# Kernel optimization log

Measured on AMD Instinct MI355X. Metric: run time of the kernel, lower is better.

The kernel has to match this reference:

```python
import jax, jax.numpy as jnp
import numpy as np

N_CLASSES = 3

def setup_inputs() -> dict:
    key = jax.random.key(0)
    k1, k2 = jax.random.split(key)
    feats = jax.random.normal(k1, (16, 1024, 1024, 3), dtype=jnp.float32)
    inst = jax.random.randint(k2, (16, 1024, 1024, 1), 0, N_CLASSES, dtype=jnp.int32)
    return {"feats": feats, "inst": inst}

def reference(feats, inst):
    # Faithful to the TF layer: for each class c, compute the GLOBAL mean of
    # feats over all masked elements (mask tiled across the 3 channels, over
    # the whole batch), then scatter that scalar back into masked positions.
    # Class masks are disjoint, so the sequential update order is benign.
    for c in range(N_CLASSES):
        mask = (inst == c)                                   # [B,H,W,1]
        maskb = jnp.broadcast_to(mask, feats.shape)          # [B,H,W,3]
        cnt = jnp.sum(maskb.astype(feats.dtype))             # scalar count (incl. channels)
        feats_mean = jnp.sum(jnp.where(maskb, feats, 0)) / cnt
        feats = jnp.where(maskb, feats_mean, feats)
    return feats
```

## Files before the change

kernel.cpp:

```cpp
#include <hip/hip_runtime.h>


#define RBLK 1024

__device__ inline double wred_d(double v) {
#pragma unroll
    for (int off = 32; off; off >>= 1) v += __shfl_down(v, off, 64);
    return v;
}
__device__ inline unsigned wred_u(unsigned v) {
#pragma unroll
    for (int off = 32; off; off >>= 1) v += __shfl_down(v, off, 64);
    return v;
}

__global__ __launch_bounds__(256) void reduce_k(const float* __restrict__ feats,
                                                const int* __restrict__ inst,
                                                double* __restrict__ psum,
                                                unsigned* __restrict__ pcnt,
                                                int npix4) {
    int tid = blockIdx.x * 256 + threadIdx.x;
    int stride = gridDim.x * 256;
    double s0 = 0.0, s1 = 0.0, s2 = 0.0;
    unsigned c0 = 0, c1 = 0, c2 = 0;
    const int4* inst4 = (const int4*)inst;
    for (int i = tid; i < npix4; i += stride) {
        int4 cls = inst4[i];
        const float4* f = (const float4*)(feats + (size_t)i * 12);
        float4 a = f[0], b = f[1], c = f[2];
        double d0 = (double)(a.x + a.y + a.z);
        double d1 = (double)(a.w + b.x + b.y);
        double d2 = (double)(b.z + b.w + c.x);
        double d3 = (double)(c.y + c.z + c.w);
        s0 += (cls.x == 0) ? d0 : 0.0;
        s1 += (cls.x == 1) ? d0 : 0.0;
        s2 += (cls.x == 2) ? d0 : 0.0;
        s0 += (cls.y == 0) ? d1 : 0.0;
        s1 += (cls.y == 1) ? d1 : 0.0;
        s2 += (cls.y == 2) ? d1 : 0.0;
        s0 += (cls.z == 0) ? d2 : 0.0;
        s1 += (cls.z == 1) ? d2 : 0.0;
        s2 += (cls.z == 2) ? d2 : 0.0;
        s0 += (cls.w == 0) ? d3 : 0.0;
        s1 += (cls.w == 1) ? d3 : 0.0;
        s2 += (cls.w == 2) ? d3 : 0.0;
        c0 += (unsigned)(cls.x == 0) + (unsigned)(cls.y == 0) +
              (unsigned)(cls.z == 0) + (unsigned)(cls.w == 0);
        c1 += (unsigned)(cls.x == 1) + (unsigned)(cls.y == 1) +
              (unsigned)(cls.z == 1) + (unsigned)(cls.w == 1);
        c2 += (unsigned)(cls.x == 2) + (unsigned)(cls.y == 2) +
              (unsigned)(cls.z == 2) + (unsigned)(cls.w == 2);
    }
    s0 = wred_d(s0); s1 = wred_d(s1); s2 = wred_d(s2);
    c0 = wred_u(c0); c1 = wred_u(c1); c2 = wred_u(c2);

    __shared__ double ls[4][3];
    __shared__ unsigned lc[4][3];
    int wid = threadIdx.x >> 6;
    int lane = threadIdx.x & 63;
    if (lane == 0) {
        ls[wid][0] = s0; ls[wid][1] = s1; ls[wid][2] = s2;
        lc[wid][0] = c0; lc[wid][1] = c1; lc[wid][2] = c2;
    }
    __syncthreads();
    if (threadIdx.x < 3) {
        int c = threadIdx.x;
        double s = ls[0][c] + ls[1][c] + ls[2][c] + ls[3][c];
        unsigned cc = lc[0][c] + lc[1][c] + lc[2][c] + lc[3][c];
        psum[blockIdx.x * 3 + c] = s;
        pcnt[blockIdx.x * 3 + c] = cc;
    }
}

__global__ __launch_bounds__(256) void finalize_k(const double* __restrict__ psum,
                                                  const unsigned* __restrict__ pcnt,
                                                  float* __restrict__ mean,
                                                  int nblk) {
    double s0 = 0.0, s1 = 0.0, s2 = 0.0;
    unsigned c0 = 0, c1 = 0, c2 = 0;
    for (int i = threadIdx.x; i < nblk; i += 256) {
        s0 += psum[i * 3 + 0]; s1 += psum[i * 3 + 1]; s2 += psum[i * 3 + 2];
        c0 += pcnt[i * 3 + 0]; c1 += pcnt[i * 3 + 1]; c2 += pcnt[i * 3 + 2];
    }
    s0 = wred_d(s0); s1 = wred_d(s1); s2 = wred_d(s2);
    c0 = wred_u(c0); c1 = wred_u(c1); c2 = wred_u(c2);

    __shared__ double ls[4][3];
    __shared__ unsigned lc[4][3];
    int wid = threadIdx.x >> 6;
    int lane = threadIdx.x & 63;
    if (lane == 0) {
        ls[wid][0] = s0; ls[wid][1] = s1; ls[wid][2] = s2;
        lc[wid][0] = c0; lc[wid][1] = c1; lc[wid][2] = c2;
    }
    __syncthreads();
    if (threadIdx.x < 3) {
        int c = threadIdx.x;
        double s = ls[0][c] + ls[1][c] + ls[2][c] + ls[3][c];
        unsigned cc = lc[0][c] + lc[1][c] + lc[2][c] + lc[3][c];
        mean[c] = (float)(s / (3.0 * (double)cc));
    }
}

__global__ __launch_bounds__(256) void scatter_k(const int* __restrict__ inst,
                                                 const float* __restrict__ mean,
                                                 float* __restrict__ out,
                                                 int npix4) {
    int i = blockIdx.x * 256 + threadIdx.x;
    if (i >= npix4) return;
    float m0 = mean[0], m1 = mean[1], m2 = mean[2];
    int4 cls = ((const int4*)inst)[i];
    float vx = (cls.x == 1) ? m1 : ((cls.x == 2) ? m2 : m0);
    float vy = (cls.y == 1) ? m1 : ((cls.y == 2) ? m2 : m0);
    float vz = (cls.z == 1) ? m1 : ((cls.z == 2) ? m2 : m0);
    float vw = (cls.w == 1) ? m1 : ((cls.w == 2) ? m2 : m0);
    float4* o = (float4*)(out + (size_t)i * 12);
    o[0] = make_float4(vx, vx, vx, vy);
    o[1] = make_float4(vy, vy, vz, vz);
    o[2] = make_float4(vz, vw, vw, vw);
}

extern "C" void kernel_launch(void* const* d_in, const int* in_sizes, int n_in,
                              void* d_out, int out_size, void* d_ws, size_t ws_size,
                              hipStream_t stream) {
    const float* feats = (const float*)d_in[0];
    const int* inst = (const int*)d_in[1];
    float* out = (float*)d_out;

    int npix = in_sizes[1];
    int npix4 = npix >> 2;

    double* psum = (double*)d_ws;
    unsigned* pcnt = (unsigned*)(psum + RBLK * 3);
    float* mean = (float*)(pcnt + RBLK * 3);

    reduce_k<<<RBLK, 256, 0, stream>>>(feats, inst, psum, pcnt, npix4);
    finalize_k<<<1, 256, 0, stream>>>(psum, pcnt, mean, RBLK);
    scatter_k<<<(npix4 + 255) / 256, 256, 0, stream>>>(inst, mean, out, npix4);
}
```

Before: 408.1 us.

## Pack class labels into byte codes and fuse finalize into scatter

During the reduction pass, the four int32 class labels per group are packed into one byte and written to workspace. The scatter pass then reads those bytes instead of re-reading the int32 labels, cutting its label traffic sixteenfold. The finalize kernel is folded into the scatter kernel: every block redundantly reduces the per-block partials before scattering, which removes one launch. The reduction grid also doubles. In exchange, the reduce pass gains an extra strided byte store, and each scatter block repeats the partial-sum reduction.

```diff
diff --git a/kernel.cpp b/kernel.cpp
--- a/kernel.cpp
+++ b/kernel.cpp
@@ -1,7 +1,7 @@
 #include <hip/hip_runtime.h>
 
 
-#define RBLK 1024
+#define RBLK 2048
 
 __device__ inline double wred_d(double v) {
 #pragma unroll
@@ -14,11 +14,12 @@
     return v;
 }
 
-__global__ __launch_bounds__(256) void reduce_k(const float* __restrict__ feats,
-                                                const int* __restrict__ inst,
-                                                double* __restrict__ psum,
-                                                unsigned* __restrict__ pcnt,
-                                                int npix4) {
+__global__ __launch_bounds__(256) void reduce_pack_k(const float* __restrict__ feats,
+                                                     const int* __restrict__ inst,
+                                                     double* __restrict__ psum,
+                                                     unsigned* __restrict__ pcnt,
+                                                     unsigned char* __restrict__ codes,
+                                                     int npix4) {
     int tid = blockIdx.x * 256 + threadIdx.x;
     int stride = gridDim.x * 256;
     double s0 = 0.0, s1 = 0.0, s2 = 0.0;
@@ -50,6 +51,8 @@
               (unsigned)(cls.z == 1) + (unsigned)(cls.w == 1);
         c2 += (unsigned)(cls.x == 2) + (unsigned)(cls.y == 2) +
               (unsigned)(cls.z == 2) + (unsigned)(cls.w == 2);
+        codes[i] = (unsigned char)((cls.x & 3) | ((cls.y & 3) << 2) |
+                                   ((cls.z & 3) << 4) | ((cls.w & 3) << 6));
     }
     s0 = wred_d(s0); s1 = wred_d(s1); s2 = wred_d(s2);
     c0 = wred_u(c0); c1 = wred_u(c1); c2 = wred_u(c2);
@@ -72,13 +75,14 @@
     }
 }
 
-__global__ __launch_bounds__(256) void finalize_k(const double* __restrict__ psum,
-                                                  const unsigned* __restrict__ pcnt,
-                                                  float* __restrict__ mean,
-                                                  int nblk) {
+__global__ __launch_bounds__(256) void mean_scatter_k(const double* __restrict__ psum,
+                                                      const unsigned* __restrict__ pcnt,
+                                                      const unsigned char* __restrict__ codes,
+                                                      float* __restrict__ out,
+                                                      int npix4) {
     double s0 = 0.0, s1 = 0.0, s2 = 0.0;
     unsigned c0 = 0, c1 = 0, c2 = 0;
-    for (int i = threadIdx.x; i < nblk; i += 256) {
+    for (int i = threadIdx.x; i < RBLK; i += 256) {
         s0 += psum[i * 3 + 0]; s1 += psum[i * 3 + 1]; s2 += psum[i * 3 + 2];
         c0 += pcnt[i * 3 + 0]; c1 += pcnt[i * 3 + 1]; c2 += pcnt[i * 3 + 2];
     }
@@ -87,6 +91,7 @@
 
     __shared__ double ls[4][3];
     __shared__ unsigned lc[4][3];
+    __shared__ float smean[3];
     int wid = threadIdx.x >> 6;
     int lane = threadIdx.x & 63;
     if (lane == 0) {
@@ -98,26 +103,25 @@
         int c = threadIdx.x;
         double s = ls[0][c] + ls[1][c] + ls[2][c] + ls[3][c];
         unsigned cc = lc[0][c] + lc[1][c] + lc[2][c] + lc[3][c];
-        mean[c] = (float)(s / (3.0 * (double)cc));
+        smean[c] = (float)(s / (3.0 * (double)cc));
     }
-}
+    __syncthreads();
+    float m0 = smean[0], m1 = smean[1], m2 = smean[2];
 
-__global__ __launch_bounds__(256) void scatter_k(const int* __restrict__ inst,
-                                                 const float* __restrict__ mean,
-                                                 float* __restrict__ out,
-                                                 int npix4) {
-    int i = blockIdx.x * 256 + threadIdx.x;
-    if (i >= npix4) return;
-    float m0 = mean[0], m1 = mean[1], m2 = mean[2];
-    int4 cls = ((const int4*)inst)[i];
-    float vx = (cls.x == 1) ? m1 : ((cls.x == 2) ? m2 : m0);
-    float vy = (cls.y == 1) ? m1 : ((cls.y == 2) ? m2 : m0);
-    float vz = (cls.z == 1) ? m1 : ((cls.z == 2) ? m2 : m0);
-    float vw = (cls.w == 1) ? m1 : ((cls.w == 2) ? m2 : m0);
-    float4* o = (float4*)(out + (size_t)i * 12);
-    o[0] = make_float4(vx, vx, vx, vy);
-    o[1] = make_float4(vy, vy, vz, vz);
-    o[2] = make_float4(vz, vw, vw, vw);
+    int tid = blockIdx.x * 256 + threadIdx.x;
+    int stride = gridDim.x * 256;
+    for (int i = tid; i < npix4; i += stride) {
+        unsigned cb = codes[i];
+        unsigned x = cb & 3, y = (cb >> 2) & 3, z = (cb >> 4) & 3, w = (cb >> 6) & 3;
+        float vx = (x == 1) ? m1 : ((x == 2) ? m2 : m0);
+        float vy = (y == 1) ? m1 : ((y == 2) ? m2 : m0);
+        float vz = (z == 1) ? m1 : ((z == 2) ? m2 : m0);
+        float vw = (w == 1) ? m1 : ((w == 2) ? m2 : m0);
+        float4* o = (float4*)(out + (size_t)i * 12);
+        o[0] = make_float4(vx, vx, vx, vy);
+        o[1] = make_float4(vy, vy, vz, vz);
+        o[2] = make_float4(vz, vw, vw, vw);
+    }
 }
 
 extern "C" void kernel_launch(void* const* d_in, const int* in_sizes, int n_in,
@@ -132,9 +136,8 @@
 
     double* psum = (double*)d_ws;
     unsigned* pcnt = (unsigned*)(psum + RBLK * 3);
-    float* mean = (float*)(pcnt + RBLK * 3);
+    unsigned char* codes = (unsigned char*)(pcnt + RBLK * 3);
 
-    reduce_k<<<RBLK, 256, 0, stream>>>(feats, inst, psum, pcnt, npix4);
-    finalize_k<<<1, 256, 0, stream>>>(psum, pcnt, mean, RBLK);
-    scatter_k<<<(npix4 + 255) / 256, 256, 0, stream>>>(inst, mean, out, npix4);
+    reduce_pack_k<<<RBLK, 256, 0, stream>>>(feats, inst, psum, pcnt, codes, npix4);
+    mean_scatter_k<<<RBLK, 256, 0, stream>>>(psum, pcnt, codes, out, npix4);
 }
```

After: 403.2 us. No clear change (-1.2%).
